# Optimization experiments

Measured on AMD Instinct MI355X. Metric: run time of the kernel, lower is better.

Reference implementation:

```python
import jax, jax.numpy as jnp
import numpy as np

B, C, HH, WW = 8, 512, 32, 32
HEADS, GROUPS, EPS = 8, 32, 1e-5


def setup_inputs() -> dict:
    key = jax.random.key(0)
    k0, k1, k2 = jax.random.split(key, 3)
    x = jax.random.normal(k0, (B, C, HH, WW), jnp.float32)
    gamma = jnp.ones((C,), jnp.float32)
    beta = jnp.zeros((C,), jnp.float32)
    # 1x1 convs modeled as (out, in) matrices; fan-in scaling keeps logits sane
    w_qkv = jax.random.normal(k1, (3 * C, C), jnp.float32) * (C ** -0.5)
    b_qkv = jnp.zeros((3 * C,), jnp.float32)
    w_proj = jax.random.normal(k2, (C, C), jnp.float32) * (C ** -0.5)
    b_proj = jnp.zeros((C,), jnp.float32)
    return {"x": x, "gamma": gamma, "beta": beta, "w_qkv": w_qkv,
            "b_qkv": b_qkv, "w_proj": w_proj, "b_proj": b_proj}


def reference(x, gamma, beta, w_qkv, b_qkv, w_proj, b_proj):
    b, c, h, w = x.shape
    S = h * w
    xr = x.reshape(b, c, S)
    # GroupNorm(32, C) over (channels_in_group, spatial)
    xg = xr.reshape(b, GROUPS, c // GROUPS, S)
    mu = xg.mean(axis=(2, 3), keepdims=True)
    var = xg.var(axis=(2, 3), keepdims=True)
    xn = ((xg - mu) * jax.lax.rsqrt(var + EPS)).reshape(b, c, S)
    xn = xn * gamma[None, :, None] + beta[None, :, None]
    # qkv 1x1 conv: (B, 3C, S)
    qkv = jnp.einsum('oc,bcs->bos', w_qkv, xn) + b_qkv[None, :, None]
    D = c // HEADS
    qkv = qkv.reshape(b, 3, HEADS, D, S)  # channel layout: (three, H, D)
    q = jnp.transpose(qkv[:, 0], (0, 1, 3, 2))  # (B, H, S, D)
    k = jnp.transpose(qkv[:, 1], (0, 1, 3, 2))
    v = jnp.transpose(qkv[:, 2], (0, 1, 3, 2))
    scale = 1.0 / float(np.sqrt(np.sqrt(D)))
    logits = jnp.einsum('bhtd,bhsd->bhts', q * scale, k * scale)  # (B,H,S,S)
    logits = logits - jnp.max(logits, axis=-1, keepdims=True)
    probs = jax.nn.softmax(logits, axis=-1)  # dropout p=0 (default)
    attn = jnp.einsum('bhts,bhsd->bhtd', probs, v)  # (B,H,S,D)
    hout = jnp.transpose(attn, (0, 1, 3, 2)).reshape(b, c, S)  # (B, H*D=C, S)
    hout = jnp.einsum('oc,bcs->bos', w_proj, hout) + b_proj[None, :, None]
    return (hout + xr).reshape(b, c, h, w)
```

## Files before the change

kernel.cpp:

```cpp
#include <hip/hip_runtime.h>
#include <hip/hip_bf16.h>

typedef __hip_bfloat16 bf16;
typedef unsigned short u16;
typedef __attribute__((ext_vector_type(8))) short bf16x8;
typedef __attribute__((ext_vector_type(4))) float f32x4;

static constexpr int Bn = 8;
static constexpr int C = 512;
static constexpr int S = 1024;
static constexpr int NH = 8;
static constexpr int HD = 64;
static constexpr int CPG = 16;
#define EPSV 1e-5f
#define QSCALE 0.18033688011112042f

__device__ __forceinline__ u16 f2bf(float f) {
    bf16 h = __float2bfloat16(f);
    return *reinterpret_cast<u16*>(&h);
}
__device__ __forceinline__ unsigned pack_bf2(float a, float b) {
    __hip_bfloat162 h = __float22bfloat162_rn(make_float2(a, b));
    return *reinterpret_cast<unsigned*>(&h);
}

__device__ __forceinline__ void async_copy16(const void* g, void* l) {
    __builtin_amdgcn_global_load_lds(
        (const __attribute__((address_space(1))) void*)g,
        (__attribute__((address_space(3))) void*)l, 16, 0, 0);
}

__global__ __launch_bounds__(256) void prep(const float* __restrict__ x,
                                            const float* __restrict__ wqkv,
                                            const float* __restrict__ wproj,
                                            float* __restrict__ stats,
                                            u16* __restrict__ wbf) {
    const int tid = threadIdx.x;
    if (blockIdx.x < 256) {
        const int bg = blockIdx.x;
        const size_t base = (size_t)bg * CPG * S;
        const int N = CPG * S;
        float sum = 0.f, sq = 0.f;
        for (int i = tid * 4; i < N; i += 1024) {
            float4 v = *reinterpret_cast<const float4*>(&x[base + i]);
            sum += v.x + v.y + v.z + v.w;
            sq += v.x * v.x + v.y * v.y + v.z * v.z + v.w * v.w;
        }
#pragma unroll
        for (int off = 32; off > 0; off >>= 1) {
            sum += __shfl_down(sum, off, 64);
            sq  += __shfl_down(sq,  off, 64);
        }
        __shared__ float s0[4], s1[4];
        if ((tid & 63) == 0) { s0[tid >> 6] = sum; s1[tid >> 6] = sq; }
        __syncthreads();
        if (tid == 0) {
            float a  = s0[0] + s0[1] + s0[2] + s0[3];
            float b2 = s1[0] + s1[1] + s1[2] + s1[3];
            float mu = a / (float)N;
            float var = fmaxf(b2 / (float)N - mu * mu, 0.f);
            stats[bg] = mu;
            stats[256 + bg] = rsqrtf(var + EPSV);
        }
    } else {
        int idx = (blockIdx.x - 256) * 1024 + tid * 4;
        float4 v;
        float sc = 1.f;
        if (idx < 1536 * 512) {
            v = *reinterpret_cast<const float4*>(&wqkv[idx]);
            if (idx < 512 * 512) sc = QSCALE;
        } else {
            v = *reinterpret_cast<const float4*>(&wproj[idx - 1536 * 512]);
        }
        u16 t[4] = {f2bf(v.x * sc), f2bf(v.y * sc), f2bf(v.z * sc), f2bf(v.w * sc)};
        *reinterpret_cast<uint2*>(&wbf[idx]) = *reinterpret_cast<uint2*>(t);
    }
}

__global__ __launch_bounds__(256) void gn_apply_t(const float* __restrict__ x,
                                                  const float* __restrict__ gamma,
                                                  const float* __restrict__ beta,
                                                  const float* __restrict__ stats,
                                                  u16* __restrict__ xnt) {
    const int b = blockIdx.z, c0 = blockIdx.y * 64, s0 = blockIdx.x * 64;
    const int tid = threadIdx.x;
    __shared__ u16 T[64 * 72];
    const float* xb = x + ((size_t)b * C + c0) * S;
#pragma unroll
    for (int i = 0; i < 4; ++i) {
        int ch = i * 256 + tid;
        int c = ch >> 4, seg = ch & 15;
        int cg = c0 + c;
        float mu = stats[b * 32 + (cg >> 4)];
        float rstd = stats[256 + b * 32 + (cg >> 4)];
        float ga = gamma[cg], be = beta[cg];
        float4 v = *reinterpret_cast<const float4*>(&xb[(size_t)c * S + s0 + seg * 4]);
        float vals[4] = {v.x, v.y, v.z, v.w};
#pragma unroll
        for (int j = 0; j < 4; ++j)
            T[(seg * 4 + j) * 72 + c] = f2bf((vals[j] - mu) * rstd * ga + be);
    }
    __syncthreads();
#pragma unroll
    for (int i = 0; i < 2; ++i) {
        int ch = i * 256 + tid;
        int r = ch >> 3, seg = ch & 7;
        uint4 val = *reinterpret_cast<const uint4*>(&T[r * 72 + seg * 8]);
        *reinterpret_cast<uint4*>(&xnt[(size_t)(b * S + s0 + r) * C + c0 + seg * 8]) = val;
    }
}

template <int MODE>
__global__ __launch_bounds__(256) void mfma_gemm(const u16* __restrict__ Wb,
                                                 const u16* __restrict__ Xt,
                                                 const float* __restrict__ bias,
                                                 const float* __restrict__ resid,
                                                 u16* __restrict__ qkvT,
                                                 u16* __restrict__ qkvV,
                                                 float* __restrict__ Yf) {
    const int K = 512;
    const int b = blockIdx.z, o0 = blockIdx.y * 128, s0 = blockIdx.x * 128;
    const int tid = threadIdx.x;
    const int lane = tid & 63, w = tid >> 6;
    const int quad = lane >> 4, l15 = lane & 15;
    const int wr = w >> 1, wc = w & 1;
    __shared__ u16 As[128 * 64];
    __shared__ u16 Bs[128 * 64];
    f32x4 acc[4][4] = {};
    const u16* Xb = Xt + (size_t)(b * S + s0) * K;
    for (int k0 = 0; k0 < K; k0 += 64) {
#pragma unroll
        for (int i = 0; i < 4; ++i) {
            int ci = w * 4 + i;
            int r = ci * 8 + (lane >> 3);
            int c = (lane & 7) ^ (r & 7);
            async_copy16(&Wb[(size_t)(o0 + r) * K + k0 + c * 8], &As[ci * 512]);
            async_copy16(&Xb[(size_t)r * K + k0 + c * 8], &Bs[ci * 512]);
        }
        __syncthreads();
#pragma unroll
        for (int kk = 0; kk < 2; ++kk) {
            bf16x8 af[4], bfr[4];
#pragma unroll
            for (int mt = 0; mt < 4; ++mt) {
                int R = wr * 64 + mt * 16 + l15;
                af[mt] = *reinterpret_cast<const bf16x8*>(
                    &As[R * 64 + (((kk * 4 + quad) ^ (R & 7)) << 3)]);
            }
#pragma unroll
            for (int nt = 0; nt < 4; ++nt) {
                int R = wc * 64 + nt * 16 + l15;
                bfr[nt] = *reinterpret_cast<const bf16x8*>(
                    &Bs[R * 64 + (((kk * 4 + quad) ^ (R & 7)) << 3)]);
            }
#pragma unroll
            for (int mt = 0; mt < 4; ++mt)
#pragma unroll
                for (int nt = 0; nt < 4; ++nt)
                    acc[mt][nt] = __builtin_amdgcn_mfma_f32_16x16x32_bf16(
                        af[mt], bfr[nt], acc[mt][nt], 0, 0, 0);
        }
        __syncthreads();
    }
    if (MODE == 1) {
#pragma unroll
        for (int mt = 0; mt < 4; ++mt) {
#pragma unroll
            for (int reg = 0; reg < 4; ++reg) {
                int o = o0 + wr * 64 + mt * 16 + quad * 4 + reg;
                float bz = bias[o];
#pragma unroll
                for (int nt = 0; nt < 4; ++nt) {
                    int s = s0 + wc * 64 + nt * 16 + l15;
                    size_t idx = (size_t)(b * C + o) * S + s;
                    Yf[idx] = acc[mt][nt][reg] + bz + resid[idx];
                }
            }
        }
    } else if (o0 < 1024) {
        float bsc = (o0 < 512) ? QSCALE : 1.f;
#pragma unroll
        for (int mt = 0; mt < 4; ++mt) {
            int o_b = o0 + wr * 64 + mt * 16 + quad * 4;
            float bz[4];
#pragma unroll
            for (int reg = 0; reg < 4; ++reg) bz[reg] = bias[o_b + reg] * bsc;
#pragma unroll
            for (int nt = 0; nt < 4; ++nt) {
                int s = s0 + wc * 64 + nt * 16 + l15;
                uint2 pk;
                pk.x = pack_bf2(acc[mt][nt][0] + bz[0], acc[mt][nt][1] + bz[1]);
                pk.y = pack_bf2(acc[mt][nt][2] + bz[2], acc[mt][nt][3] + bz[3]);
                *reinterpret_cast<uint2*>(&qkvT[(size_t)(b * S + s) * 1024 + o_b]) = pk;
            }
        }
    } else {
#pragma unroll
        for (int mt = 0; mt < 4; ++mt) {
#pragma unroll
            for (int reg = 0; reg < 4; ++reg) {
                int o = o0 - 1024 + wr * 64 + mt * 16 + quad * 4 + reg;
                float bz = bias[o + 1024];
#pragma unroll
                for (int nt = 0; nt < 4; ++nt) {
                    int s = s0 + wc * 64 + nt * 16 + l15;
                    qkvV[(size_t)(b * 512 + o) * S + s] = f2bf(acc[mt][nt][reg] + bz);
                }
            }
        }
    }
}

__global__ __launch_bounds__(256) void attn_mfma(const u16* __restrict__ qkvT,
                                                 const u16* __restrict__ qkvV,
                                                 u16* __restrict__ houtt) {
    const int b = blockIdx.z, h = blockIdx.y, q0 = blockIdx.x * 64;
    const int tid = threadIdx.x;
    const int lane = tid & 63, w = tid >> 6;
    const int quad = lane >> 4, l15 = lane & 15;
    __shared__ u16 qs[64 * 64];
    __shared__ u16 ks[2][64 * 64];
    __shared__ u16 vs[2][64 * 64];
    __shared__ u16 ps[64 * 72];

    const u16* qrow = qkvT + (size_t)(b * S + q0) * 1024 + h * HD;
    const u16* krow = qkvT + (size_t)b * S * 1024 + 512 + h * HD;
    const u16* vrow = qkvV + (size_t)(b * 512 + h * HD) * S;

#pragma unroll
    for (int i = 0; i < 2; ++i) {
        int ci = w * 2 + i;
        int r = ci * 8 + (lane >> 3);
        int c = (lane & 7) ^ (r & 7);
        async_copy16(&qrow[(size_t)r * 1024 + c * 8], &qs[ci * 512]);
        async_copy16(&krow[(size_t)r * 1024 + c * 8], &ks[0][ci * 512]);
        async_copy16(&vrow[(size_t)r * S + c * 8], &vs[0][ci * 512]);
    }
    __syncthreads();
    const int Rq = w * 16 + l15;
    bf16x8 qfrag[2];
#pragma unroll
    for (int kk = 0; kk < 2; ++kk)
        qfrag[kk] = *reinterpret_cast<const bf16x8*>(
            &qs[Rq * 64 + (((kk * 4 + quad) ^ (Rq & 7)) << 3)]);

    f32x4 o_acc[4] = {};
    float l_i = 0.f;

    for (int t = 0; t < 16; ++t) {
        const int cur = t & 1, nxt = cur ^ 1;
        if (t < 15) {
            int kt = (t + 1) * 64;
#pragma unroll
            for (int i = 0; i < 2; ++i) {
                int ci = w * 2 + i;
                int r = ci * 8 + (lane >> 3);
                int c = (lane & 7) ^ (r & 7);
                async_copy16(&krow[(size_t)(kt + r) * 1024 + c * 8], &ks[nxt][ci * 512]);
                async_copy16(&vrow[(size_t)r * S + kt + c * 8], &vs[nxt][ci * 512]);
            }
        }
        f32x4 s_acc[4] = {};
#pragma unroll
        for (int kk = 0; kk < 2; ++kk)
#pragma unroll
            for (int mt = 0; mt < 4; ++mt) {
                int Rk = mt * 16 + l15;
                bf16x8 kf = *reinterpret_cast<const bf16x8*>(
                    &ks[cur][Rk * 64 + (((kk * 4 + quad) ^ (Rk & 7)) << 3)]);
                s_acc[mt] = __builtin_amdgcn_mfma_f32_16x16x32_bf16(
                    kf, qfrag[kk], s_acc[mt], 0, 0, 0);
            }
        float rs = 0.f;
#pragma unroll
        for (int mt = 0; mt < 4; ++mt) {
            float p0 = __builtin_amdgcn_exp2f(s_acc[mt][0]);
            float p1 = __builtin_amdgcn_exp2f(s_acc[mt][1]);
            float p2 = __builtin_amdgcn_exp2f(s_acc[mt][2]);
            float p3 = __builtin_amdgcn_exp2f(s_acc[mt][3]);
            rs += (p0 + p1) + (p2 + p3);
            uint2 pk;
            pk.x = pack_bf2(p0, p1);
            pk.y = pack_bf2(p2, p3);
            *reinterpret_cast<uint2*>(&ps[Rq * 72 + mt * 16 + quad * 4]) = pk;
        }
        l_i += rs;
#pragma unroll
        for (int kk = 0; kk < 2; ++kk) {
            bf16x8 pf = *reinterpret_cast<const bf16x8*>(
                &ps[Rq * 72 + kk * 32 + quad * 8]);
#pragma unroll
            for (int mt = 0; mt < 4; ++mt) {
                int Rv = mt * 16 + l15;
                bf16x8 vf = *reinterpret_cast<const bf16x8*>(
                    &vs[cur][Rv * 64 + (((kk * 4 + quad) ^ (Rv & 7)) << 3)]);
                o_acc[mt] = __builtin_amdgcn_mfma_f32_16x16x32_bf16(
                    vf, pf, o_acc[mt], 0, 0, 0);
            }
        }
        __syncthreads();
    }
    l_i += __shfl_xor(l_i, 16, 64);
    l_i += __shfl_xor(l_i, 32, 64);
    float inv = 1.f / l_i;
    u16* orow = houtt + (size_t)(b * S + q0 + w * 16 + l15) * 512 + h * HD;
#pragma unroll
    for (int mt = 0; mt < 4; ++mt) {
        uint2 pk;
        pk.x = pack_bf2(o_acc[mt][0] * inv, o_acc[mt][1] * inv);
        pk.y = pack_bf2(o_acc[mt][2] * inv, o_acc[mt][3] * inv);
        *reinterpret_cast<uint2*>(&orow[mt * 16 + quad * 4]) = pk;
    }
}

extern "C" void kernel_launch(void* const* d_in, const int* in_sizes, int n_in,
                              void* d_out, int out_size, void* d_ws, size_t ws_size,
                              hipStream_t stream) {
    const float* x      = (const float*)d_in[0];
    const float* gamma  = (const float*)d_in[1];
    const float* beta   = (const float*)d_in[2];
    const float* w_qkv  = (const float*)d_in[3];
    const float* b_qkv  = (const float*)d_in[4];
    const float* w_proj = (const float*)d_in[5];
    const float* b_proj = (const float*)d_in[6];
    float* out = (float*)d_out;

    char* ws = (char*)d_ws;
    float* stats = (float*)ws;
    u16* wbf   = (u16*)(ws + 4096);
    u16* xnt   = (u16*)(ws + 4096 + 2097152);
    u16* qkvT  = (u16*)(ws + 4096 + 2097152 + 8388608);
    u16* qkvV  = (u16*)(ws + 4096 + 2097152 + 8388608 + 16777216);
    u16* houtt = xnt;

    prep<<<1280, 256, 0, stream>>>(x, w_qkv, w_proj, stats, wbf);
    gn_apply_t<<<dim3(16, 8, Bn), 256, 0, stream>>>(x, gamma, beta, stats, xnt);
    mfma_gemm<0><<<dim3(8, 12, Bn), 256, 0, stream>>>(
        wbf, xnt, b_qkv, nullptr, qkvT, qkvV, nullptr);
    attn_mfma<<<dim3(16, NH, Bn), 256, 0, stream>>>(qkvT, qkvV, houtt);
    mfma_gemm<1><<<dim3(8, 4, Bn), 256, 0, stream>>>(
        wbf + 1536 * 512, houtt, b_proj, x, nullptr, nullptr, out);
}
```

Measured before the change: 172.6 us.

## Switch attention to 32x32x16 MFMA with 128-query tiles per block

Result: faster. 160.0 us (-7.3%).

```diff
diff --git a/kernel.cpp b/kernel.cpp
--- a/kernel.cpp
+++ b/kernel.cpp
@@ -5,6 +5,7 @@
 typedef unsigned short u16;
 typedef __attribute__((ext_vector_type(8))) short bf16x8;
 typedef __attribute__((ext_vector_type(4))) float f32x4;
+typedef __attribute__((ext_vector_type(16))) float f32x16;
 
 static constexpr int Bn = 8;
 static constexpr int C = 512;
@@ -214,38 +215,36 @@
 __global__ __launch_bounds__(256) void attn_mfma(const u16* __restrict__ qkvT,
                                                  const u16* __restrict__ qkvV,
                                                  u16* __restrict__ houtt) {
-    const int b = blockIdx.z, h = blockIdx.y, q0 = blockIdx.x * 64;
+    const int b = blockIdx.z, h = blockIdx.y, q0 = blockIdx.x * 128;
     const int tid = threadIdx.x;
     const int lane = tid & 63, w = tid >> 6;
-    const int quad = lane >> 4, l15 = lane & 15;
-    __shared__ u16 qs[64 * 64];
+    const int l31 = lane & 31, half = lane >> 5;
     __shared__ u16 ks[2][64 * 64];
     __shared__ u16 vs[2][64 * 64];
-    __shared__ u16 ps[64 * 72];
-
-    const u16* qrow = qkvT + (size_t)(b * S + q0) * 1024 + h * HD;
+    __shared__ u16 ps[128 * 68];
+
+    const u16* qrow = qkvT + (size_t)(b * S + q0 + w * 32 + l31) * 1024 + h * HD;
     const u16* krow = qkvT + (size_t)b * S * 1024 + 512 + h * HD;
     const u16* vrow = qkvV + (size_t)(b * 512 + h * HD) * S;
+
+    bf16x8 qfrag[4];
+#pragma unroll
+    for (int kk = 0; kk < 4; ++kk)
+        qfrag[kk] = *reinterpret_cast<const bf16x8*>(&qrow[kk * 16 + half * 8]);
 
 #pragma unroll
     for (int i = 0; i < 2; ++i) {
         int ci = w * 2 + i;
         int r = ci * 8 + (lane >> 3);
         int c = (lane & 7) ^ (r & 7);
-        async_copy16(&qrow[(size_t)r * 1024 + c * 8], &qs[ci * 512]);
         async_copy16(&krow[(size_t)r * 1024 + c * 8], &ks[0][ci * 512]);
         async_copy16(&vrow[(size_t)r * S + c * 8], &vs[0][ci * 512]);
     }
     __syncthreads();
-    const int Rq = w * 16 + l15;
-    bf16x8 qfrag[2];
-#pragma unroll
-    for (int kk = 0; kk < 2; ++kk)
-        qfrag[kk] = *reinterpret_cast<const bf16x8*>(
-            &qs[Rq * 64 + (((kk * 4 + quad) ^ (Rq & 7)) << 3)]);
-
-    f32x4 o_acc[4] = {};
+
+    f32x16 o_acc[2] = {};
     float l_i = 0.f;
+    const int prow = (w * 32 + l31) * 68;
 
     for (int t = 0; t < 16; ++t) {
         const int cur = t & 1, nxt = cur ^ 1;
@@ -260,57 +259,69 @@
                 async_copy16(&vrow[(size_t)r * S + kt + c * 8], &vs[nxt][ci * 512]);
             }
         }
-        f32x4 s_acc[4] = {};
-#pragma unroll
-        for (int kk = 0; kk < 2; ++kk)
-#pragma unroll
-            for (int mt = 0; mt < 4; ++mt) {
-                int Rk = mt * 16 + l15;
+        f32x16 s_acc[2] = {};
+#pragma unroll
+        for (int mt = 0; mt < 2; ++mt) {
+            int r = mt * 32 + l31;
+#pragma unroll
+            for (int kk = 0; kk < 4; ++kk) {
+                int c8 = kk * 2 + half;
                 bf16x8 kf = *reinterpret_cast<const bf16x8*>(
-                    &ks[cur][Rk * 64 + (((kk * 4 + quad) ^ (Rk & 7)) << 3)]);
-                s_acc[mt] = __builtin_amdgcn_mfma_f32_16x16x32_bf16(
+                    &ks[cur][r * 64 + ((c8 ^ (r & 7)) << 3)]);
+                s_acc[mt] = __builtin_amdgcn_mfma_f32_32x32x16_bf16(
                     kf, qfrag[kk], s_acc[mt], 0, 0, 0);
             }
+        }
         float rs = 0.f;
 #pragma unroll
-        for (int mt = 0; mt < 4; ++mt) {
-            float p0 = __builtin_amdgcn_exp2f(s_acc[mt][0]);
-            float p1 = __builtin_amdgcn_exp2f(s_acc[mt][1]);
-            float p2 = __builtin_amdgcn_exp2f(s_acc[mt][2]);
-            float p3 = __builtin_amdgcn_exp2f(s_acc[mt][3]);
-            rs += (p0 + p1) + (p2 + p3);
-            uint2 pk;
-            pk.x = pack_bf2(p0, p1);
-            pk.y = pack_bf2(p2, p3);
-            *reinterpret_cast<uint2*>(&ps[Rq * 72 + mt * 16 + quad * 4]) = pk;
-        }
+        for (int mt = 0; mt < 2; ++mt)
+#pragma unroll
+            for (int g = 0; g < 4; ++g) {
+                float p0 = __builtin_amdgcn_exp2f(s_acc[mt][g * 4 + 0]);
+                float p1 = __builtin_amdgcn_exp2f(s_acc[mt][g * 4 + 1]);
+                float p2 = __builtin_amdgcn_exp2f(s_acc[mt][g * 4 + 2]);
+                float p3 = __builtin_amdgcn_exp2f(s_acc[mt][g * 4 + 3]);
+                rs += (p0 + p1) + (p2 + p3);
+                uint2 pk;
+                pk.x = pack_bf2(p0, p1);
+                pk.y = pack_bf2(p2, p3);
+                *reinterpret_cast<uint2*>(&ps[prow + mt * 32 + g * 8 + half * 4]) = pk;
+            }
         l_i += rs;
-#pragma unroll
-        for (int kk = 0; kk < 2; ++kk) {
-            bf16x8 pf = *reinterpret_cast<const bf16x8*>(
-                &ps[Rq * 72 + kk * 32 + quad * 8]);
-#pragma unroll
-            for (int mt = 0; mt < 4; ++mt) {
-                int Rv = mt * 16 + l15;
+        bf16x8 pf[4];
+#pragma unroll
+        for (int kk = 0; kk < 4; ++kk) {
+            union { uint2 u[2]; bf16x8 v; } u8;
+            u8.u[0] = *reinterpret_cast<const uint2*>(&ps[prow + kk * 16 + half * 8]);
+            u8.u[1] = *reinterpret_cast<const uint2*>(&ps[prow + kk * 16 + half * 8 + 4]);
+            pf[kk] = u8.v;
+        }
+#pragma unroll
+        for (int nt = 0; nt < 2; ++nt) {
+            int rv = nt * 32 + l31;
+#pragma unroll
+            for (int kk = 0; kk < 4; ++kk) {
+                int c8 = kk * 2 + half;
                 bf16x8 vf = *reinterpret_cast<const bf16x8*>(
-                    &vs[cur][Rv * 64 + (((kk * 4 + quad) ^ (Rv & 7)) << 3)]);
-                o_acc[mt] = __builtin_amdgcn_mfma_f32_16x16x32_bf16(
-                    vf, pf, o_acc[mt], 0, 0, 0);
+                    &vs[cur][rv * 64 + ((c8 ^ (rv & 7)) << 3)]);
+                o_acc[nt] = __builtin_amdgcn_mfma_f32_32x32x16_bf16(
+                    vf, pf[kk], o_acc[nt], 0, 0, 0);
             }
         }
         __syncthreads();
     }
-    l_i += __shfl_xor(l_i, 16, 64);
     l_i += __shfl_xor(l_i, 32, 64);
     float inv = 1.f / l_i;
-    u16* orow = houtt + (size_t)(b * S + q0 + w * 16 + l15) * 512 + h * HD;
-#pragma unroll
-    for (int mt = 0; mt < 4; ++mt) {
-        uint2 pk;
-        pk.x = pack_bf2(o_acc[mt][0] * inv, o_acc[mt][1] * inv);
-        pk.y = pack_bf2(o_acc[mt][2] * inv, o_acc[mt][3] * inv);
-        *reinterpret_cast<uint2*>(&orow[mt * 16 + quad * 4]) = pk;
-    }
+    u16* orow = houtt + (size_t)(b * S + q0 + w * 32 + l31) * 512 + h * HD;
+#pragma unroll
+    for (int nt = 0; nt < 2; ++nt)
+#pragma unroll
+        for (int g = 0; g < 4; ++g) {
+            uint2 pk;
+            pk.x = pack_bf2(o_acc[nt][g * 4 + 0] * inv, o_acc[nt][g * 4 + 1] * inv);
+            pk.y = pack_bf2(o_acc[nt][g * 4 + 2] * inv, o_acc[nt][g * 4 + 3] * inv);
+            *reinterpret_cast<uint2*>(&orow[nt * 32 + g * 8 + half * 4]) = pk;
+        }
 }
 
 extern "C" void kernel_launch(void* const* d_in, const int* in_sizes, int n_in,
@@ -337,7 +348,7 @@
     gn_apply_t<<<dim3(16, 8, Bn), 256, 0, stream>>>(x, gamma, beta, stats, xnt);
     mfma_gemm<0><<<dim3(8, 12, Bn), 256, 0, stream>>>(
         wbf, xnt, b_qkv, nullptr, qkvT, qkvV, nullptr);
-    attn_mfma<<<dim3(16, NH, Bn), 256, 0, stream>>>(qkvT, qkvV, houtt);
+    attn_mfma<<<dim3(8, NH, Bn), 256, 0, stream>>>(qkvT, qkvV, houtt);
     mfma_gemm<1><<<dim3(8, 4, Bn), 256, 0, stream>>>(
         wbf + 1536 * 512, houtt, b_proj, x, nullptr, nullptr, out);
 }
```
